# Kernel tuning notes

Hardware: AMD Instinct MI355X
Metric: run time of the kernel (lower is better)

The kernel has to match this reference:

```python
import jax, jax.numpy as jnp
import numpy as np

N_TOKENS = 65536
EMBED_DIM = 1024
NUM_EXPERTS = 8
TOP_K = 2
NOISE_EPS = 0.2


def setup_inputs() -> dict:
    key = jax.random.key(0)
    k_x, k_eps, k_wg, k_wn = jax.random.split(key, 4)
    x = jax.random.normal(k_x, (N_TOKENS, EMBED_DIM), dtype=jnp.float32)
    eps = jax.random.normal(k_eps, (N_TOKENS, NUM_EXPERTS), dtype=jnp.float32)
    # nn.init.normal_(std=1.0) on both weights
    w_gate = jax.random.normal(k_wg, (EMBED_DIM, NUM_EXPERTS), dtype=jnp.float32)
    w_noise = jax.random.normal(k_wn, (EMBED_DIM, NUM_EXPERTS), dtype=jnp.float32)
    return {"x": x, "eps": eps, "w_gate": w_gate, "w_noise": w_noise}


def reference(x, eps, w_gate, w_noise):
    # skinny GEMMs: [N, D] @ [D, E] -> [N, E]
    clean_logits = x @ w_gate
    raw_noise_stddev = x @ w_noise
    noise_stddev = jax.nn.softplus(raw_noise_stddev) + NOISE_EPS
    noisy_logits = clean_logits + noise_stddev * eps

    # top-k over the tiny expert dim, softmax over the k selected logits
    top_k_logits, indices = jax.lax.top_k(noisy_logits, TOP_K)  # [N, K]
    top_k_gates = jax.nn.softmax(top_k_logits, axis=-1)

    # scatter gates back into dense [N, E]
    n = noisy_logits.shape[0]
    rows = jnp.arange(n)[:, None]
    gates = jnp.zeros_like(noisy_logits).at[rows, indices].set(top_k_gates)

    # load-balancing aux loss
    probs = jax.nn.softmax(clean_logits, axis=-1)
    P = probs.mean(axis=0)                             # [E]
    f = (gates > 0).astype(x.dtype).mean(axis=0)       # [E]
    aux_loss = NUM_EXPERTS * jnp.sum(P * f)
    return gates, aux_loss
```

## Files before the change

### kernel.cpp

```cpp
#include <hip/hip_runtime.h>
#include <math.h>


#define N_TOKENS   65536
#define EMBED_DIM  1024
#define NE         8
#define BROWS      64
#define CHUNK      64
#define NCHUNK     (EMBED_DIM / CHUNK)
#define QSTRIDE    260
#define NSLOT      64
#define NOISE_EPS  0.2f

#define AS1(p) (const __attribute__((address_space(1))) void*)(p)
#define AS3(p) (__attribute__((address_space(3))) void*)(p)

__global__ __launch_bounds__(256, 4)
void router_kernel(const float* __restrict__ x,
                   const float* __restrict__ eps,
                   const float* __restrict__ wg,
                   const float* __restrict__ wn,
                   float* __restrict__ gates,
                   float* __restrict__ acc ) {
    __shared__ float tile[2][16 * QSTRIDE];

    const int t    = threadIdx.x;
    const int lane = t & 63;
    const int w    = __builtin_amdgcn_readfirstlane(t >> 6);
    const long rowbase = (long)blockIdx.x * BROWS;

    const int srow = lane >> 4;
    const int scol = (lane & 15) * 4;

    const int tb = (lane >> 2) * QSTRIDE + (lane & 3) * 64 + w * 16;

    float accg[NE], accn[NE];
#pragma unroll
    for (int e = 0; e < NE; ++e) { accg[e] = 0.f; accn[e] = 0.f; }

#pragma unroll
    for (int i = 0; i < 4; ++i) {
        const int q = w * 4 + i;
        const float* gp = x + (rowbase + q * 4 + srow) * (long)EMBED_DIM + scol;
        __builtin_amdgcn_global_load_lds(AS1(gp), AS3(&tile[0][q * QSTRIDE]), 16, 0, 0);
    }
    __syncthreads();

#pragma unroll 1
    for (int c = 0; c < NCHUNK; ++c) {
        const int b = c & 1;
        if (c + 1 < NCHUNK) {
#pragma unroll
            for (int i = 0; i < 4; ++i) {
                const int q = w * 4 + i;
                const float* gp = x + (rowbase + q * 4 + srow) * (long)EMBED_DIM
                                  + (c + 1) * CHUNK + scol;
                __builtin_amdgcn_global_load_lds(AS1(gp), AS3(&tile[b ^ 1][q * QSTRIDE]),
                                                 16, 0, 0);
            }
        }

        const float* wgc = wg + ((long)c * CHUNK + w * 16) * NE;
        const float* wnc = wn + ((long)c * CHUNK + w * 16) * NE;
        float4 xv[4];
#pragma unroll
        for (int j = 0; j < 4; ++j)
            xv[j] = *(const float4*)&tile[b][tb + j * 4];
#pragma unroll
        for (int j = 0; j < 4; ++j) {
            const float xa[4] = { xv[j].x, xv[j].y, xv[j].z, xv[j].w };
#pragma unroll
            for (int q = 0; q < 4; ++q) {
                const int k = j * 4 + q;
#pragma unroll
                for (int e = 0; e < NE; ++e) {
                    accg[e] = fmaf(xa[q], wgc[k * NE + e], accg[e]);
                    accn[e] = fmaf(xa[q], wnc[k * NE + e], accn[e]);
                }
            }
        }
        __syncthreads();
    }

    float* part = (float*)tile;
    if (w != 0) {
#pragma unroll
        for (int e = 0; e < NE; ++e) {
            part[((w - 1) * BROWS + lane) * 16 + e]      = accg[e];
            part[((w - 1) * BROWS + lane) * 16 + NE + e] = accn[e];
        }
    }
    __syncthreads();
    if (w != 0) return;

#pragma unroll
    for (int v = 0; v < 3; ++v)
#pragma unroll
        for (int e = 0; e < NE; ++e) {
            accg[e] += part[(v * BROWS + lane) * 16 + e];
            accn[e] += part[(v * BROWS + lane) * 16 + NE + e];
        }

    const long row = rowbase + lane;
    const float* er = eps + row * NE;
    float4 ev0 = *(const float4*)(er);
    float4 ev1 = *(const float4*)(er + 4);
    float epsv[NE] = { ev0.x, ev0.y, ev0.z, ev0.w, ev1.x, ev1.y, ev1.z, ev1.w };

    float noisy[NE];
#pragma unroll
    for (int e = 0; e < NE; ++e) {
        float r = accn[e];
        float sp = fmaxf(r, 0.f) + log1pf(expf(-fabsf(r)));
        noisy[e] = accg[e] + (sp + NOISE_EPS) * epsv[e];
    }

    int i1 = 0; float v1 = noisy[0];
#pragma unroll
    for (int e = 1; e < NE; ++e) if (noisy[e] > v1) { v1 = noisy[e]; i1 = e; }
    int i2 = -1; float v2 = -INFINITY;
#pragma unroll
    for (int e = 0; e < NE; ++e) if (e != i1 && noisy[e] > v2) { v2 = noisy[e]; i2 = e; }

    float bb = expf(v2 - v1);
    float g2 = bb / (1.f + bb);
    float g1 = 1.f - g2;

    float* gr = gates + row * NE;
    float ov[NE];
#pragma unroll
    for (int e = 0; e < NE; ++e)
        ov[e] = (e == i1) ? g1 : ((e == i2) ? g2 : 0.f);
    *(float4*)(gr)     = make_float4(ov[0], ov[1], ov[2], ov[3]);
    *(float4*)(gr + 4) = make_float4(ov[4], ov[5], ov[6], ov[7]);

    float mx = accg[0];
#pragma unroll
    for (int e = 1; e < NE; ++e) mx = fmaxf(mx, accg[e]);
    float p[NE]; float s = 0.f;
#pragma unroll
    for (int e = 0; e < NE; ++e) { p[e] = expf(accg[e] - mx); s += p[e]; }
    float inv = 1.f / s;

    float vals[16];
#pragma unroll
    for (int e = 0; e < NE; ++e) {
        vals[e]      = p[e] * inv;
        vals[NE + e] = ((i1 == e) ? 1.f : 0.f) + ((i2 == e && g2 > 0.f) ? 1.f : 0.f);
    }
#pragma unroll
    for (int off = 32; off > 0; off >>= 1)
#pragma unroll
        for (int i = 0; i < 16; ++i)
            vals[i] += __shfl_xor(vals[i], off, 64);

    if (lane == 0) {
        float* slot = acc + (blockIdx.x & (NSLOT - 1)) * 16;
#pragma unroll
        for (int i = 0; i < 16; ++i)
            atomicAdd(&slot[i], vals[i]);
    }
}

__global__ void finalize_kernel(const float* __restrict__ acc,
                                float* __restrict__ out_aux) {
    __shared__ float s[16];
    const int t = threadIdx.x;
    if (t < 16) {
        float v = 0.f;
        for (int j = 0; j < NSLOT; ++j) v += acc[j * 16 + t];
        s[t] = v;
    }
    __syncthreads();
    if (t == 0) {
        const float invn = 1.f / (float)N_TOKENS;
        float aux = 0.f;
#pragma unroll
        for (int e = 0; e < NE; ++e)
            aux += (s[e] * invn) * (s[NE + e] * invn);
        *out_aux = (float)NE * aux;
    }
}

extern "C" void kernel_launch(void* const* d_in, const int* in_sizes, int n_in,
                              void* d_out, int out_size, void* d_ws, size_t ws_size,
                              hipStream_t stream) {
    const float* x   = (const float*)d_in[0];
    const float* eps = (const float*)d_in[1];
    const float* wg  = (const float*)d_in[2];
    const float* wn  = (const float*)d_in[3];
    float* out = (float*)d_out;
    float* acc = (float*)d_ws;

    hipMemsetAsync(d_ws, 0, NSLOT * 16 * sizeof(float), stream);

    router_kernel<<<dim3(N_TOKENS / BROWS), dim3(256), 0, stream>>>(
        x, eps, wg, wn, out, acc);
    finalize_kernel<<<dim3(1), dim3(64), 0, stream>>>(acc, out + (out_size - 1));
}
```

Baseline: 409.3 us.

## Use single-buffered 256-wide chunks with per-row loads instead of double-buffered 64-wide

Replaces the double-buffered 64-column staging with a single LDS tile holding 64 rows by 256 columns, loaded as full contiguous row segments per wavefront. This cuts the number of chunk iterations and barriers from 16 to 4 and makes each global load a contiguous 1 KB row segment. Occupancy hint drops from 4 to 2 blocks per SIMD. Loads for the next chunk are no longer overlapped with compute, so memory latency is exposed at each barrier.

New measurement: 413.5 us. Within noise of the previous version (+1.0%).

```diff
diff --git a/kernel.cpp b/kernel.cpp
--- a/kernel.cpp
+++ b/kernel.cpp
@@ -6,69 +6,51 @@
 #define EMBED_DIM  1024
 #define NE         8
 #define BROWS      64
-#define CHUNK      64
-#define NCHUNK     (EMBED_DIM / CHUNK)
-#define QSTRIDE    260
+#define CHUNK      256
+#define NCH        (EMBED_DIM / CHUNK)
+#define RSTRIDE    260
 #define NSLOT      64
 #define NOISE_EPS  0.2f
 
 #define AS1(p) (const __attribute__((address_space(1))) void*)(p)
 #define AS3(p) (__attribute__((address_space(3))) void*)(p)
 
-__global__ __launch_bounds__(256, 4)
+__global__ __launch_bounds__(256, 2)
 void router_kernel(const float* __restrict__ x,
                    const float* __restrict__ eps,
                    const float* __restrict__ wg,
                    const float* __restrict__ wn,
                    float* __restrict__ gates,
                    float* __restrict__ acc ) {
-    __shared__ float tile[2][16 * QSTRIDE];
+    __shared__ float tile[BROWS * RSTRIDE];
 
     const int t    = threadIdx.x;
     const int lane = t & 63;
     const int w    = __builtin_amdgcn_readfirstlane(t >> 6);
     const long rowbase = (long)blockIdx.x * BROWS;
 
-    const int srow = lane >> 4;
-    const int scol = (lane & 15) * 4;
-
-    const int tb = (lane >> 2) * QSTRIDE + (lane & 3) * 64 + w * 16;
-
     float accg[NE], accn[NE];
 #pragma unroll
     for (int e = 0; e < NE; ++e) { accg[e] = 0.f; accn[e] = 0.f; }
 
 #pragma unroll
-    for (int i = 0; i < 4; ++i) {
-        const int q = w * 4 + i;
-        const float* gp = x + (rowbase + q * 4 + srow) * (long)EMBED_DIM + scol;
-        __builtin_amdgcn_global_load_lds(AS1(gp), AS3(&tile[0][q * QSTRIDE]), 16, 0, 0);
+    for (int i = 0; i < 16; ++i) {
+        const int r = w * 16 + i;
+        const float* gp = x + (rowbase + r) * (long)EMBED_DIM + lane * 4;
+        __builtin_amdgcn_global_load_lds(AS1(gp), AS3(&tile[r * RSTRIDE]), 16, 0, 0);
     }
-    __syncthreads();
 
-#pragma unroll 1
-    for (int c = 0; c < NCHUNK; ++c) {
-        const int b = c & 1;
-        if (c + 1 < NCHUNK) {
 #pragma unroll
-            for (int i = 0; i < 4; ++i) {
-                const int q = w * 4 + i;
-                const float* gp = x + (rowbase + q * 4 + srow) * (long)EMBED_DIM
-                                  + (c + 1) * CHUNK + scol;
-                __builtin_amdgcn_global_load_lds(AS1(gp), AS3(&tile[b ^ 1][q * QSTRIDE]),
-                                                 16, 0, 0);
-            }
-        }
+    for (int c = 0; c < NCH; ++c) {
+        __syncthreads();
 
-        const float* wgc = wg + ((long)c * CHUNK + w * 16) * NE;
-        const float* wnc = wn + ((long)c * CHUNK + w * 16) * NE;
-        float4 xv[4];
-#pragma unroll
-        for (int j = 0; j < 4; ++j)
-            xv[j] = *(const float4*)&tile[b][tb + j * 4];
-#pragma unroll
-        for (int j = 0; j < 4; ++j) {
-            const float xa[4] = { xv[j].x, xv[j].y, xv[j].z, xv[j].w };
+        const float4* trow = (const float4*)tile + lane * (RSTRIDE / 4) + w * 16;
+        const float* wgc = wg + ((long)c * CHUNK + w * 64) * NE;
+        const float* wnc = wn + ((long)c * CHUNK + w * 64) * NE;
+#pragma unroll 4
+        for (int j = 0; j < 16; ++j) {
+            float4 xv = trow[j];
+            const float xa[4] = { xv.x, xv.y, xv.z, xv.w };
 #pragma unroll
             for (int q = 0; q < 4; ++q) {
                 const int k = j * 4 + q;
@@ -80,9 +62,20 @@
             }
         }
         __syncthreads();
+
+        if (c + 1 < NCH) {
+#pragma unroll
+            for (int i = 0; i < 16; ++i) {
+                const int r = w * 16 + i;
+                const float* gp = x + (rowbase + r) * (long)EMBED_DIM
+                                  + (c + 1) * CHUNK + lane * 4;
+                __builtin_amdgcn_global_load_lds(AS1(gp), AS3(&tile[r * RSTRIDE]),
+                                                 16, 0, 0);
+            }
+        }
     }
 
-    float* part = (float*)tile;
+    float* part = tile;
     if (w != 0) {
 #pragma unroll
         for (int e = 0; e < NE; ++e) {
```
